# Kernel optimization log

Hardware: AMD Instinct MI355X
Metric: run time of the kernel (lower is better)

The kernel has to match this reference:

```python
import jax, jax.numpy as jnp
import numpy as np

IN_C = 256
INTER_C = 64  # in_c // k, k=4
B, H, W = 8, 32, 32
N_TERMS = 5   # numSeriesTerms; numTraceSamples = 1


def setup_inputs():
    key = jax.random.key(0)
    ks = jax.random.split(key, 10)
    s = 0.05
    return {
        "x": jax.random.normal(ks[0], (B, IN_C, H, W), jnp.float32),
        "Wq": jax.random.normal(ks[1], (INTER_C, IN_C), jnp.float32) * s,
        "bq": jax.random.normal(ks[2], (INTER_C,), jnp.float32) * s,
        "Wk": jax.random.normal(ks[3], (INTER_C, IN_C), jnp.float32) * s,
        "bk": jax.random.normal(ks[4], (INTER_C,), jnp.float32) * s,
        "Wc": jax.random.normal(ks[5], (2 * INTER_C,), jnp.float32) * s,
        "Wv": jax.random.normal(ks[6], (IN_C, IN_C), jnp.float32) * s,
        "bv": jax.random.normal(ks[7], (IN_C,), jnp.float32) * s,
        "gamma": jnp.full((1,), 0.5, jnp.float32),
        "u": jax.random.normal(ks[8], (B, IN_C, H, W), jnp.float32),
    }


def _attention(x, Wq, bq, Wk, bk, Wc, Wv, bv, gamma):
    # Attention_concat.forward. concat_conv is a bias-free linear map over the
    # channel concat, so energy[i,j] = <Wc[:ic], q_i> + <Wc[ic:], k_j> exactly.
    b, c, h, w = x.shape
    n = h * w
    xf = x.reshape(b, c, n)                                   # [B,C,N]
    q = jnp.einsum('oc,bcn->bon', Wq, xf) + bq[None, :, None]  # [B,ic,N]
    k = jnp.einsum('oc,bcn->bon', Wk, xf) + bk[None, :, None]  # [B,ic,N]
    ic = Wq.shape[0]
    eq = jnp.einsum('c,bcn->bn', Wc[:ic], q)                  # [B,N]
    ek = jnp.einsum('c,bcn->bn', Wc[ic:], k)                  # [B,N]
    attn = (eq[:, :, None] + ek[:, None, :]) / n              # energy/(H*W), [B,N,N]
    v = jnp.einsum('oc,bcn->bon', Wv, xf) + bv[None, :, None]  # [B,C,N]
    out = jnp.einsum('bcn,bnm->bcm', v, attn).reshape(b, c, h, w)
    return gamma * out + x


def _forward(x, Wq, bq, Wk, bk, Wc, Wv, bv, gamma, u):
    att = lambda z, g: _attention(z, Wq, bq, Wk, bk, Wc, Wv, bv, g)
    # turbulance_hook: runs under torch.no_grad and rescales gamma in-place
    res = att(x, gamma)
    turbu = att(x * 1.0000001, gamma)
    lip = jnp.linalg.norm(turbu - res) / jnp.linalg.norm(x * 1.0000001 - x)
    factor = jax.lax.stop_gradient(jnp.where(lip > 0.9, 0.9 / lip, 1.0))
    gamma_eff = gamma * factor
    Fx, vjp_fn = jax.vjp(lambda z: att(z, gamma_eff), x)
    # power_series_matrix_logarithm_trace: Hutchinson estimate of
    # tr(log(I+J)) ~= sum_j (-1)^{j+1}/j * u^T J^j u, 1 probe, 5 terms
    b = x.shape[0]
    uf = u.reshape(b, -1)
    vcur = u
    tr = jnp.zeros((b,), x.dtype)
    for j in range(1, N_TERMS + 1):
        vcur = vjp_fn(vcur)[0]                 # u^T J^j via repeated vjp
        dot = jnp.sum(vcur.reshape(b, -1) * uf, axis=1)
        tr = tr + ((-1.0) ** (j + 1) / j) * dot
    return x + Fx, tr


def reference(x, Wq, bq, Wk, bk, Wc, Wv, bv, gamma, u):
    return _forward(x, Wq, bq, Wk, bk, Wc, Wv, bv, gamma, u)
```

## Files before the change

### kernel.cpp

```cpp
#include <hip/hip_runtime.h>
#include <math.h>

#define NB 8
#define NC 256
#define NN 1024
#define NICH 64

#define WS_AQ    0
#define WS_AK    256
#define WS_CQ    512
#define WS_CK    513
#define WS_GE    514
#define WS_MOM   520
#define WS_SX    1024
#define WS_XE    3072
#define WS_XK    5120
#define WS_T1P   7424
#define WS_T2P   7488
#define WS_VSU   7680
#define WS_UE    9728
#define WS_VEU   11776
#define WS_CAQ   13824
#define WS_CAK   15872
#define WS_CUAK  17920
#define WS_STAT  20480
#define STAT_STRIDE 2560
#define ST_EQ    0
#define ST_EK    1024
#define ST_SV    2048
#define ST_SVE   2304
#define WS_MAQ   40960
#define WS_MAK   49152
#define WS_EQP   57344
#define WS_EKP   319488
#define WS_MAQP  581632
#define WS_MAKP  843776
#define WS_SX2P  1105920
#define WS_UUP   1106176

__device__ __forceinline__ float dot4(const float4& a, const float4& b) {
    return a.x * b.x + a.y * b.y + a.z * b.z + a.w * b.w;
}
__device__ __forceinline__ float sum4(const float4& a) {
    return a.x + a.y + a.z + a.w;
}

__global__ void k1(const float* __restrict__ x, const float* __restrict__ u,
                   const float* __restrict__ Wq, const float* __restrict__ bq,
                   const float* __restrict__ Wk, const float* __restrict__ bk,
                   const float* __restrict__ Wc, float* __restrict__ ws) {
    const int bid = blockIdx.x;
    const int b = bid >> 5, g = bid & 31;
    const int t = threadIdx.x;
    const int c0 = g * 8;
    const int wid = t >> 6, lane = t & 63;
    __shared__ float aql[8], akl[8];
    __shared__ float sxw[8][4];
    {
        const int c = t >> 5, i = t & 31;
        float a = Wc[i] * Wq[i * NC + c0 + c] + Wc[i + 32] * Wq[(i + 32) * NC + c0 + c];
        float k = Wc[64 + i] * Wk[i * NC + c0 + c] + Wc[96 + i] * Wk[(i + 32) * NC + c0 + c];
        for (int off = 16; off > 0; off >>= 1) {
            a += __shfl_down(a, off, 32);
            k += __shfl_down(k, off, 32);
        }
        if (i == 0) {
            aql[c] = a; akl[c] = k;
            ws[WS_AQ + c0 + c] = a;
            ws[WS_AK + c0 + c] = k;
        }
    }
    if (t < 64) {
        float p = Wc[t] * bq[t], r = Wc[64 + t] * bk[t];
        for (int off = 32; off > 0; off >>= 1) {
            p += __shfl_down(p, off, 64);
            r += __shfl_down(r, off, 64);
        }
        if (t == 0) { ws[WS_CQ] = p; ws[WS_CK] = r; }
    }
    __syncthreads();
    const float4* xb4 = (const float4*)(x + ((size_t)b * NC + c0) * NN);
    const float4* ub4 = (const float4*)(u + ((size_t)b * NC + c0) * NN);
    float4 eqp = {0.f, 0.f, 0.f, 0.f}, ekp = {0.f, 0.f, 0.f, 0.f};
    float4 map = {0.f, 0.f, 0.f, 0.f}, mkp = {0.f, 0.f, 0.f, 0.f};
#pragma unroll
    for (int c = 0; c < 8; ++c) {
        float4 xv = xb4[c * 256 + t];
        float4 uv = ub4[c * 256 + t];
        float a = aql[c], k = akl[c];
        eqp.x += a * xv.x; eqp.y += a * xv.y; eqp.z += a * xv.z; eqp.w += a * xv.w;
        ekp.x += k * xv.x; ekp.y += k * xv.y; ekp.z += k * xv.z; ekp.w += k * xv.w;
        map.x += a * uv.x; map.y += a * uv.y; map.z += a * uv.z; map.w += a * uv.w;
        mkp.x += k * uv.x; mkp.y += k * uv.y; mkp.z += k * uv.z; mkp.w += k * uv.w;
        float xs = sum4(xv);
        for (int off = 32; off > 0; off >>= 1) xs += __shfl_down(xs, off, 64);
        if (lane == 0) sxw[c][wid] = xs;
    }
    __syncthreads();
    if (t < 8) ws[WS_SX + b * NC + c0 + t] = sxw[t][0] + sxw[t][1] + sxw[t][2] + sxw[t][3];
    size_t pb = (size_t)bid * 1024;
    ((float4*)(ws + WS_EQP + pb))[t]  = eqp;
    ((float4*)(ws + WS_EKP + pb))[t]  = ekp;
    ((float4*)(ws + WS_MAQP + pb))[t] = map;
    ((float4*)(ws + WS_MAKP + pb))[t] = mkp;
}

__global__ void k2(float* __restrict__ ws) {
    const int bid = blockIdx.x;
    const int b = bid >> 2, qc = bid & 3;
    const int t = threadIdx.x;
    const int quarter = t >> 6, tn = t & 63;
    const int n4 = qc * 64 + tn;
    __shared__ float4 qb[4][4][64];
    float4 e4 = {0.f, 0.f, 0.f, 0.f}, k4 = {0.f, 0.f, 0.f, 0.f};
    float4 ma4 = {0.f, 0.f, 0.f, 0.f}, mk4 = {0.f, 0.f, 0.f, 0.f};
#pragma unroll
    for (int gg = 0; gg < 8; ++gg) {
        size_t pb = (size_t)(b * 32 + quarter * 8 + gg) * 1024;
        float4 v0 = ((const float4*)(ws + WS_EQP + pb))[n4];
        float4 v1 = ((const float4*)(ws + WS_EKP + pb))[n4];
        float4 v2 = ((const float4*)(ws + WS_MAQP + pb))[n4];
        float4 v3 = ((const float4*)(ws + WS_MAKP + pb))[n4];
        e4.x += v0.x; e4.y += v0.y; e4.z += v0.z; e4.w += v0.w;
        k4.x += v1.x; k4.y += v1.y; k4.z += v1.z; k4.w += v1.w;
        ma4.x += v2.x; ma4.y += v2.y; ma4.z += v2.z; ma4.w += v2.w;
        mk4.x += v3.x; mk4.y += v3.y; mk4.z += v3.z; mk4.w += v3.w;
    }
    qb[0][quarter][tn] = e4; qb[1][quarter][tn] = k4;
    qb[2][quarter][tn] = ma4; qb[3][quarter][tn] = mk4;
    __syncthreads();
    if (t < 64) {
        const float cq = ws[WS_CQ], ck = ws[WS_CK];
        float4 e = qb[0][0][t], kk = qb[1][0][t], ma = qb[2][0][t], mk = qb[3][0][t];
        for (int qq = 1; qq < 4; ++qq) {
            float4 a0 = qb[0][qq][t], a1 = qb[1][qq][t], a2 = qb[2][qq][t], a3 = qb[3][qq][t];
            e.x += a0.x; e.y += a0.y; e.z += a0.z; e.w += a0.w;
            kk.x += a1.x; kk.y += a1.y; kk.z += a1.z; kk.w += a1.w;
            ma.x += a2.x; ma.y += a2.y; ma.z += a2.z; ma.w += a2.w;
            mk.x += a3.x; mk.y += a3.y; mk.z += a3.z; mk.w += a3.w;
        }
        e.x += cq; e.y += cq; e.z += cq; e.w += cq;
        kk.x += ck; kk.y += ck; kk.z += ck; kk.w += ck;
        float* st = ws + WS_STAT + b * STAT_STRIDE;
        ((float4*)(st + ST_EQ))[n4] = e;
        ((float4*)(st + ST_EK))[n4] = kk;
        ((float4*)(ws + WS_MAQ + b * NN))[n4] = ma;
        ((float4*)(ws + WS_MAK + b * NN))[n4] = mk;
        float d0 = sum4(e);
        float d1 = sum4(kk);
        float d2 = dot4(kk, kk);
        float d3 = dot4(e, kk);
        for (int off = 32; off > 0; off >>= 1) {
            d0 += __shfl_down(d0, off, 64);
            d1 += __shfl_down(d1, off, 64);
            d2 += __shfl_down(d2, off, 64);
            d3 += __shfl_down(d3, off, 64);
        }
        if (t == 0) {
            ws[WS_MOM + bid * 4 + 0] = d0;
            ws[WS_MOM + bid * 4 + 1] = d1;
            ws[WS_MOM + bid * 4 + 2] = d2;
            ws[WS_MOM + bid * 4 + 3] = d3;
        }
    }
}

__global__ void k3(const float* __restrict__ x, const float* __restrict__ u,
                   float* __restrict__ ws) {
    const int bid = blockIdx.x;
    const int b = bid >> 5, g = bid & 31;
    const int t = threadIdx.x;
    const int c0 = g * 8;
    const int wid = t >> 6, lane = t & 63;
    __shared__ float wv8[8][8][4];
    __shared__ float accw[2][4];
    const float* st = ws + WS_STAT + b * STAT_STRIDE;
    float4 e4  = ((const float4*)(st + ST_EQ))[t];
    float4 k4v = ((const float4*)(st + ST_EK))[t];
    float4 ma4 = ((const float4*)(ws + WS_MAQ + b * NN))[t];
    float4 mk4 = ((const float4*)(ws + WS_MAK + b * NN))[t];
    const float4* xb4 = (const float4*)(x + ((size_t)b * NC + c0) * NN);
    const float4* ub4 = (const float4*)(u + ((size_t)b * NC + c0) * NN);
    float x2a = 0.f, uua = 0.f;
#pragma unroll
    for (int c = 0; c < 8; ++c) {
        float4 xv = xb4[c * 256 + t];
        float4 uv = ub4[c * 256 + t];
        float d[8];
        d[0] = dot4(xv, e4);
        d[1] = dot4(xv, k4v);
        d[2] = sum4(uv);
        d[3] = dot4(uv, e4);
        d[4] = dot4(uv, k4v);
        d[5] = dot4(xv, ma4);
        d[6] = dot4(xv, mk4);
        d[7] = dot4(uv, mk4);
        x2a += dot4(xv, xv);
        uua += dot4(uv, uv);
        for (int off = 32; off > 0; off >>= 1)
            for (int m = 0; m < 8; ++m) d[m] += __shfl_down(d[m], off, 64);
        if (lane == 0) for (int m = 0; m < 8; ++m) wv8[c][m][wid] = d[m];
    }
    for (int off = 32; off > 0; off >>= 1) {
        x2a += __shfl_down(x2a, off, 64);
        uua += __shfl_down(uua, off, 64);
    }
    if (lane == 0) { accw[0][wid] = x2a; accw[1][wid] = uua; }
    __syncthreads();
    if (t < 8) {
        int c = t;
        float v[8];
        for (int m = 0; m < 8; ++m)
            v[m] = wv8[c][m][0] + wv8[c][m][1] + wv8[c][m][2] + wv8[c][m][3];
        ws[WS_XE   + b * NC + c0 + c] = v[0];
        ws[WS_XK   + b * NC + c0 + c] = v[1];
        ws[WS_VSU  + b * NC + c0 + c] = v[2];
        ws[WS_UE   + b * NC + c0 + c] = v[3];
        ws[WS_VEU  + b * NC + c0 + c] = v[4];
        ws[WS_CAQ  + b * NC + c0 + c] = v[5];
        ws[WS_CAK  + b * NC + c0 + c] = v[6];
        ws[WS_CUAK + b * NC + c0 + c] = v[7];
    }
    if (t == 0) {
        ws[WS_SX2P + bid] = accw[0][0] + accw[0][1] + accw[0][2] + accw[0][3];
        ws[WS_UUP + bid]  = accw[1][0] + accw[1][1] + accw[1][2] + accw[1][3];
    }
}

__global__ void ksv(const float* __restrict__ Wv, const float* __restrict__ bv,
                    float* __restrict__ ws) {
    const int bid = blockIdx.x;
    const int b = bid >> 3, oc = bid & 7;
    const int t = threadIdx.x;
    const int o_sub = t >> 3, ks = t & 7;
    const int o = oc * 32 + o_sub;
    __shared__ float sxl[NC], xel[NC];
    __shared__ float T1s[32], T2s[32];
    sxl[t] = ws[WS_SX + b * NC + t];
    xel[t] = ws[WS_XE + b * NC + t];
    __syncthreads();
    float Seq = 0.f, Sek = 0.f, Sek2 = 0.f;
    for (int q = 0; q < 4; ++q) {
        Seq  += ws[WS_MOM + (b * 4 + q) * 4 + 0];
        Sek  += ws[WS_MOM + (b * 4 + q) * 4 + 1];
        Sek2 += ws[WS_MOM + (b * 4 + q) * 4 + 2];
    }
    const float cq = ws[WS_CQ], ck = ws[WS_CK];
    float wsx = 0.f, wxe = 0.f;
    const float4* wrow = (const float4*)(Wv + (size_t)o * NC);
#pragma unroll
    for (int i = 0; i < 8; ++i) {
        float4 w4 = wrow[i * 8 + ks];
        int k = i * 32 + ks * 4;
        wsx += w4.x * sxl[k] + w4.y * sxl[k + 1] + w4.z * sxl[k + 2] + w4.w * sxl[k + 3];
        wxe += w4.x * xel[k] + w4.y * xel[k + 1] + w4.z * xel[k + 2] + w4.w * xel[k + 3];
    }
    for (int off = 4; off > 0; off >>= 1) {
        wsx += __shfl_down(wsx, off, 8);
        wxe += __shfl_down(wxe, off, 8);
    }
    if (ks == 0) {
        float bvc = bv[o];
        float Sv  = wsx + (float)NN * bvc;
        float SvL = wsx;
        float Sve = wxe + bvc * Seq;
        float* st = ws + WS_STAT + b * STAT_STRIDE;
        st[ST_SV + o] = Sv; st[ST_SVE + o] = Sve;
        float A = 2.f * Sve - bvc * Seq - cq * Sv;
        float sx = sxl[o];
        float xk = ws[WS_XK + b * NC + o];
        float xkL = xk - ck * sx;
        float T1c = A * sx + Sv * xkL + SvL * xk;
        float SP  = Sek - (float)NN * ck;
        float SP2 = Sek2 - 2.f * ck * Sek + (float)NN * ck * ck;
        float SPQ = Sek2 - ck * Sek;
        float T2c = (float)NN * A * A + Sv * Sv * SP2 + SvL * SvL * Sek2
                  + 2.f * A * Sv * SP + 2.f * A * SvL * Sek + 2.f * Sv * SvL * SPQ;
        T1s[o_sub] = T1c; T2s[o_sub] = T2c;
    }
    __syncthreads();
    if (t == 0) {
        float t1 = 0.f, t2 = 0.f;
        for (int i = 0; i < 32; ++i) { t1 += T1s[i]; t2 += T2s[i]; }
        ws[WS_T1P + bid] = t1;
        ws[WS_T2P + bid] = t2;
    }
}

__global__ void kiter(
        const float* __restrict__ Wv, const float* __restrict__ bv,
        const float* __restrict__ gamma, float* __restrict__ ws,
        float* __restrict__ out) {
    const int b = blockIdx.x;
    const int t = threadIdx.x;
    const int o = t & 255, q = t >> 8;
    const int wid4 = o >> 6, lane = t & 63;
    __shared__ unsigned int Wlds[128 * 256];
    __shared__ float VV[2 * NC];
    __shared__ float redPR[2 * 1024];
    __shared__ float dred[9][4];
    __shared__ float gred0[4];
    __shared__ float gredT[2];
    __shared__ float sge;
#pragma unroll 4
    for (int r = 0; r < 32; ++r) {
        int c = r * 8 + q * 2;
        float w0 = Wv[(size_t)c * NC + o];
        float w1 = Wv[(size_t)(c + 1) * NC + o];
        unsigned int b0 = __float_as_uint(w0);
        unsigned int b1 = __float_as_uint(w1);
        b0 = (b0 + 0x7FFFu + ((b0 >> 16) & 1u)) >> 16;
        b1 = (b1 + 0x7FFFu + ((b1 >> 16) & 1u)) & 0xFFFF0000u;
        Wlds[(r * 4 + q) * 256 + o] = b0 | b1;
    }
    {
        float a = 0.f, b1 = 0.f, c1 = 0.f;
        if (t < 256) a = ws[WS_SX2P + t];
        if (t < 64) { b1 = ws[WS_T1P + t]; c1 = ws[WS_T2P + t]; }
        for (int off = 32; off > 0; off >>= 1) {
            a  += __shfl_down(a,  off, 64);
            b1 += __shfl_down(b1, off, 64);
            c1 += __shfl_down(c1, off, 64);
        }
        if (t < 256 && lane == 0) gred0[t >> 6] = a;
        if (t == 0) { gredT[0] = b1; gredT[1] = c1; }
    }
    __syncthreads();
    if (t == 0) {
        float S1 = gred0[0] + gred0[1] + gred0[2] + gred0[3];
        float T1 = gredT[0];
        float T2 = gredT[1];
        float inv = gamma[0] * (1.f / (float)NN);
        float dd = S1 + 2.f * inv * T1 + inv * inv * T2;
        float lip = sqrtf(dd / S1);
        float ge = gamma[0] * ((lip > 0.9f) ? (0.9f / lip) : 1.f);
        sge = ge;
        if (b == 0) ws[WS_GE] = ge;
    }
    __syncthreads();
    const float s = sge * (1.f / (float)NN);
    float Svl_r = 0.f, sxl_r = 0.f, xkl_r = 0.f, caql_r = 0.f, cakl_r = 0.f,
          Uel_r = 0.f, Vsul_r = 0.f, bvl_r = 0.f, aql_r = 0.f, akl_r = 0.f,
          veu_r = 0.f, cuak_r = 0.f, vsreg = 0.f, vereg = 0.f;
    if (t < 256) {
        const float* st = ws + WS_STAT + b * STAT_STRIDE;
        Svl_r  = st[ST_SV + t];
        sxl_r  = ws[WS_SX   + b * NC + t];
        xkl_r  = ws[WS_XK   + b * NC + t];
        caql_r = ws[WS_CAQ  + b * NC + t];
        cakl_r = ws[WS_CAK  + b * NC + t];
        Uel_r  = ws[WS_UE   + b * NC + t];
        Vsul_r = ws[WS_VSU  + b * NC + t];
        veu_r  = ws[WS_VEU  + b * NC + t];
        cuak_r = ws[WS_CUAK + b * NC + t];
        aql_r  = ws[WS_AQ + t];
        akl_r  = ws[WS_AK + t];
        bvl_r  = bv[t];
        vsreg = Vsul_r; vereg = veu_r;
        VV[2 * t] = vsreg; VV[2 * t + 1] = vereg;
    }
    float Seq = 0.f, Sek = 0.f, Sekq = 0.f;
    for (int qq = 0; qq < 4; ++qq) {
        Seq  += ws[WS_MOM + (b * 4 + qq) * 4 + 0];
        Sek  += ws[WS_MOM + (b * 4 + qq) * 4 + 1];
        Sekq += ws[WS_MOM + (b * 4 + qq) * 4 + 3];
    }
    float uu = 0.f;
    for (int g = 0; g < 32; ++g) uu += ws[WS_UUP + b * 32 + g];
    __syncthreads();
    if (t < 256) {
        float d[8] = {Svl_r * cuak_r, aql_r * Vsul_r, akl_r * Vsul_r, akl_r * Uel_r,
                      Svl_r * Vsul_r, Svl_r * veu_r,  Svl_r * aql_r,  Svl_r * akl_r};
        for (int off = 32; off > 0; off >>= 1)
            for (int m = 0; m < 8; ++m) d[m] += __shfl_down(d[m], off, 64);
        if (lane == 0) for (int m = 0; m < 8; ++m) dred[m][wid4] = d[m];
    }
    __syncthreads();
    float g2a = 0.f, aqVsu = 0.f, akVsu = 0.f, akUe = 0.f, SvVsu = 0.f, SvVeu = 0.f,
          Svaq = 0.f, Svak = 0.f;
    if (t < 256) {
        g2a   = dred[0][0] + dred[0][1] + dred[0][2] + dred[0][3];
        aqVsu = dred[1][0] + dred[1][1] + dred[1][2] + dred[1][3];
        akVsu = dred[2][0] + dred[2][1] + dred[2][2] + dred[2][3];
        akUe  = dred[3][0] + dred[3][1] + dred[3][2] + dred[3][3];
        SvVsu = dred[4][0] + dred[4][1] + dred[4][2] + dred[4][3];
        SvVeu = dred[5][0] + dred[5][1] + dred[5][2] + dred[5][3];
        Svaq  = dred[6][0] + dred[6][1] + dred[6][2] + dred[6][3];
        Svak  = dred[7][0] + dred[7][1] + dred[7][2] + dred[7][3];
    }
    __syncthreads();
    const float lam = 1.f + s * Svak;
    float alpha = 1.f, beta = 0.f, gam = 0.f;
    float SxAcc = 0.f, XkAcc = 0.f, CakAcc = 0.f;
    float dot = uu, tr = 0.f;
    const float coef[5] = {1.f, -0.5f, 1.f / 3.f, -0.25f, 0.2f};
    for (int j = 0; j < 5; ++j) {
        float pa = 0.f, ra = 0.f;
#pragma unroll
        for (int ii = 0; ii < 32; ++ii) {
            int i = q * 32 + ii;
            unsigned int w = Wlds[i * 256 + o];
            float4 vv = ((const float4*)VV)[i];
            float wlo = __uint_as_float(w << 16);
            float whi = __uint_as_float(w & 0xFFFF0000u);
            pa += wlo * vv.x + whi * vv.z;
            ra += wlo * vv.y + whi * vv.w;
        }
        redPR[2 * t] = pa; redPR[2 * t + 1] = ra;
        __syncthreads();
        float Pv = 0.f, Rv = 0.f;
        if (t < 256) {
            Pv = s * (redPR[2 * t] + redPR[2 * (t + 256)] + redPR[2 * (t + 512)] + redPR[2 * (t + 768)]);
            Rv = s * (redPR[2 * t + 1] + redPR[2 * (t + 256) + 1] + redPR[2 * (t + 512) + 1] + redPR[2 * (t + 768) + 1]);
            float d[9];
            d[0] = Svl_r * Pv;
            d[1] = Svl_r * Rv;
            d[2] = bvl_r * vsreg;
            d[3] = sxl_r * Pv;
            d[4] = xkl_r * Pv;
            d[5] = caql_r * Pv;
            d[6] = cakl_r * Pv;
            d[7] = Uel_r * Pv;
            d[8] = Vsul_r * Rv;
            for (int off = 32; off > 0; off >>= 1)
                for (int m = 0; m < 9; ++m) d[m] += __shfl_down(d[m], off, 64);
            if (lane == 0) for (int m = 0; m < 9; ++m) dred[m][wid4] = d[m];
        }
        __syncthreads();
        if (t < 256) {
            float sm[9];
            for (int m = 0; m < 9; ++m) sm[m] = dred[m][0] + dred[m][1] + dred[m][2] + dred[m][3];
            const float svP = sm[0], svR = sm[1], bvVs = sm[2], sxP = sm[3], xkP = sm[4],
                        caqP = sm[5], cakP = sm[6], ueP = sm[7], vsuR = sm[8];
            const float sB = s * bvVs;
            float St  = s * (alpha * SvVsu + beta * (float)NN + gam * Seq  + Svaq * SxAcc);
            float tek = s * (alpha * SvVeu + beta * Sek        + gam * Sekq + Svaq * XkAcc);
            float uta = s * (alpha * g2a   + beta * akVsu      + gam * akUe + Svaq * CakAcc);
            dot += ueP + caqP + sB * aqVsu + uta + vsuR;
            tr  += coef[j] * dot;
            float nVs = vsreg + Pv * Seq  + aql_r * (sxP + (float)NN * sB) + akl_r * St  + Rv * (float)NN;
            float nVe = vereg + Pv * Sekq + aql_r * (xkP + sB * Sek)       + akl_r * tek + Rv * Sek;
            vsreg = nVs; vereg = nVe;
            VV[2 * t] = nVs; VV[2 * t + 1] = nVe;
            SxAcc  = lam * SxAcc  + sxP;
            XkAcc  = lam * XkAcc  + xkP;
            CakAcc = lam * CakAcc + cakP;
            beta = lam * beta + Svaq * sB + svR;
            gam  = lam * gam + svP;
            alpha *= lam;
        }
        __syncthreads();
    }
    if (t == 0) out[2097152 + b] = tr;
}

__global__ void kout0(const float* __restrict__ x, const float* __restrict__ ws,
                      float* __restrict__ out) {
    int bid = blockIdx.x;
    int b = bid >> 8, c = bid & 255, t = threadIdx.x;
    float ge = ws[WS_GE] * (1.f / (float)NN);
    const float* st = ws + WS_STAT + b * STAT_STRIDE;
    float sv = st[ST_SV + c], sve = st[ST_SVE + c];
    float4 ek4 = ((const float4*)(st + ST_EK))[t];
    size_t i4 = (size_t)bid * 256 + t;
    float4 x4 = ((const float4*)x)[i4];
    float4 o;
    o.x = 2.f * x4.x + ge * (sve + ek4.x * sv);
    o.y = 2.f * x4.y + ge * (sve + ek4.y * sv);
    o.z = 2.f * x4.z + ge * (sve + ek4.z * sv);
    o.w = 2.f * x4.w + ge * (sve + ek4.w * sv);
    ((float4*)out)[i4] = o;
}

extern "C" void kernel_launch(void* const* d_in, const int* in_sizes, int n_in,
                              void* d_out, int out_size, void* d_ws, size_t ws_size,
                              hipStream_t stream) {
    const float* x     = (const float*)d_in[0];
    const float* Wq    = (const float*)d_in[1];
    const float* bq    = (const float*)d_in[2];
    const float* Wk    = (const float*)d_in[3];
    const float* bk    = (const float*)d_in[4];
    const float* Wc    = (const float*)d_in[5];
    const float* Wv    = (const float*)d_in[6];
    const float* bv    = (const float*)d_in[7];
    const float* gamma = (const float*)d_in[8];
    const float* u     = (const float*)d_in[9];
    float* out = (float*)d_out;
    float* ws  = (float*)d_ws;

    k1   <<<dim3(256),  dim3(256),  0, stream>>>(x, u, Wq, bq, Wk, bk, Wc, ws);
    k2   <<<dim3(32),   dim3(256),  0, stream>>>(ws);
    k3   <<<dim3(256),  dim3(256),  0, stream>>>(x, u, ws);
    ksv  <<<dim3(64),   dim3(256),  0, stream>>>(Wv, bv, ws);
    kiter<<<dim3(8),    dim3(1024), 0, stream>>>(Wv, bv, gamma, ws, out);
    kout0<<<dim3(2048), dim3(256),  0, stream>>>(x, ws, out);
}
```

Before: 55.15 us.

## Fuse six kernels into one cooperative megakernel with grid syncs

Replaces the six separate launches with a single cooperative kernel of 256 blocks. Phases are separated by grid.sync(), and their shared memory is reused through one union buffer. The serial iteration phase now runs on 256 threads per block instead of 1024, with Wv staged into LDS as packed bf16 using a different layout. This removes launch gaps between the small kernels, but costs grid-wide barriers and less parallelism in the iteration and output phases, since the final output pass now runs on 256 blocks rather than 2048.

```diff
diff --git a/kernel.cpp b/kernel.cpp
--- a/kernel.cpp
+++ b/kernel.cpp
@@ -1,5 +1,8 @@
 #include <hip/hip_runtime.h>
+#include <hip/hip_cooperative_groups.h>
 #include <math.h>
+
+namespace cg = cooperative_groups;
 
 #define NB 8
 #define NC 256
@@ -44,432 +47,446 @@
 __device__ __forceinline__ float sum4(const float4& a) {
     return a.x + a.y + a.z + a.w;
 }
-
-__global__ void k1(const float* __restrict__ x, const float* __restrict__ u,
-                   const float* __restrict__ Wq, const float* __restrict__ bq,
-                   const float* __restrict__ Wk, const float* __restrict__ bk,
-                   const float* __restrict__ Wc, float* __restrict__ ws) {
+__device__ __forceinline__ unsigned int bf16lo(float v) {
+    unsigned int u = __float_as_uint(v);
+    return (u + 0x7FFFu + ((u >> 16) & 1u)) >> 16;
+}
+__device__ __forceinline__ unsigned int bf16hi(float v) {
+    unsigned int u = __float_as_uint(v);
+    return (u + 0x7FFFu + ((u >> 16) & 1u)) & 0xFFFF0000u;
+}
+
+struct SMemP5 {
+    unsigned int Wlds2[256][128];
+    float VV[512];
+    float redM[256][8];
+    float dred[9][4];
+    float gred0[4];
+    float gredT[2];
+    float sge;
+};
+struct SMemP1 { float aql[8], akl[8]; float sxw[8][4]; };
+struct SMemP2 { float4 qb[4][4][64]; };
+struct SMemP3 { float wv8[8][8][4]; float accw[2][4]; };
+struct SMemP4 { float sxl[NC], xel[NC]; float T1s[32], T2s[32]; };
+
+__global__ void __launch_bounds__(256) mega(
+        const float* __restrict__ x, const float* __restrict__ u,
+        const float* __restrict__ Wq, const float* __restrict__ bq,
+        const float* __restrict__ Wk, const float* __restrict__ bk,
+        const float* __restrict__ Wc, const float* __restrict__ Wv,
+        const float* __restrict__ bv, const float* __restrict__ gamma,
+        float* __restrict__ ws, float* __restrict__ out) {
+    cg::grid_group grid = cg::this_grid();
+    __shared__ __align__(16) unsigned char smem_raw[sizeof(SMemP5)];
     const int bid = blockIdx.x;
-    const int b = bid >> 5, g = bid & 31;
     const int t = threadIdx.x;
-    const int c0 = g * 8;
     const int wid = t >> 6, lane = t & 63;
-    __shared__ float aql[8], akl[8];
-    __shared__ float sxw[8][4];
+
     {
-        const int c = t >> 5, i = t & 31;
-        float a = Wc[i] * Wq[i * NC + c0 + c] + Wc[i + 32] * Wq[(i + 32) * NC + c0 + c];
-        float k = Wc[64 + i] * Wk[i * NC + c0 + c] + Wc[96 + i] * Wk[(i + 32) * NC + c0 + c];
-        for (int off = 16; off > 0; off >>= 1) {
-            a += __shfl_down(a, off, 32);
-            k += __shfl_down(k, off, 32);
-        }
-        if (i == 0) {
-            aql[c] = a; akl[c] = k;
-            ws[WS_AQ + c0 + c] = a;
-            ws[WS_AK + c0 + c] = k;
-        }
+        SMemP1& S = *(SMemP1*)smem_raw;
+        const int b = bid >> 5, g = bid & 31;
+        const int c0 = g * 8;
+        {
+            const int c = t >> 5, i = t & 31;
+            float a = Wc[i] * Wq[i * NC + c0 + c] + Wc[i + 32] * Wq[(i + 32) * NC + c0 + c];
+            float k = Wc[64 + i] * Wk[i * NC + c0 + c] + Wc[96 + i] * Wk[(i + 32) * NC + c0 + c];
+            for (int off = 16; off > 0; off >>= 1) {
+                a += __shfl_down(a, off, 32);
+                k += __shfl_down(k, off, 32);
+            }
+            if (i == 0) {
+                S.aql[c] = a; S.akl[c] = k;
+                ws[WS_AQ + c0 + c] = a;
+                ws[WS_AK + c0 + c] = k;
+            }
+        }
+        if (t < 64) {
+            float p = Wc[t] * bq[t], r = Wc[64 + t] * bk[t];
+            for (int off = 32; off > 0; off >>= 1) {
+                p += __shfl_down(p, off, 64);
+                r += __shfl_down(r, off, 64);
+            }
+            if (t == 0) { ws[WS_CQ] = p; ws[WS_CK] = r; }
+        }
+        __syncthreads();
+        const float4* xb4 = (const float4*)(x + ((size_t)b * NC + c0) * NN);
+        const float4* ub4 = (const float4*)(u + ((size_t)b * NC + c0) * NN);
+        float4 eqp = {0.f, 0.f, 0.f, 0.f}, ekp = {0.f, 0.f, 0.f, 0.f};
+        float4 map = {0.f, 0.f, 0.f, 0.f}, mkp = {0.f, 0.f, 0.f, 0.f};
+#pragma unroll
+        for (int c = 0; c < 8; ++c) {
+            float4 xv = xb4[c * 256 + t];
+            float4 uv = ub4[c * 256 + t];
+            float a = S.aql[c], k = S.akl[c];
+            eqp.x += a * xv.x; eqp.y += a * xv.y; eqp.z += a * xv.z; eqp.w += a * xv.w;
+            ekp.x += k * xv.x; ekp.y += k * xv.y; ekp.z += k * xv.z; ekp.w += k * xv.w;
+            map.x += a * uv.x; map.y += a * uv.y; map.z += a * uv.z; map.w += a * uv.w;
+            mkp.x += k * uv.x; mkp.y += k * uv.y; mkp.z += k * uv.z; mkp.w += k * uv.w;
+            float xs = sum4(xv);
+            for (int off = 32; off > 0; off >>= 1) xs += __shfl_down(xs, off, 64);
+            if (lane == 0) S.sxw[c][wid] = xs;
+        }
+        __syncthreads();
+        if (t < 8) ws[WS_SX + b * NC + c0 + t] = S.sxw[t][0] + S.sxw[t][1] + S.sxw[t][2] + S.sxw[t][3];
+        size_t pb = (size_t)bid * 1024;
+        ((float4*)(ws + WS_EQP + pb))[t]  = eqp;
+        ((float4*)(ws + WS_EKP + pb))[t]  = ekp;
+        ((float4*)(ws + WS_MAQP + pb))[t] = map;
+        ((float4*)(ws + WS_MAKP + pb))[t] = mkp;
     }
-    if (t < 64) {
-        float p = Wc[t] * bq[t], r = Wc[64 + t] * bk[t];
+    grid.sync();
+
+    if (bid < 32) {
+        SMemP2& S = *(SMemP2*)smem_raw;
+        const int b = bid >> 2, qc = bid & 3;
+        const int quarter = t >> 6, tn = t & 63;
+        const int n4 = qc * 64 + tn;
+        float4 e4 = {0.f, 0.f, 0.f, 0.f}, k4 = {0.f, 0.f, 0.f, 0.f};
+        float4 ma4 = {0.f, 0.f, 0.f, 0.f}, mk4 = {0.f, 0.f, 0.f, 0.f};
+#pragma unroll
+        for (int gg = 0; gg < 8; ++gg) {
+            size_t pb = (size_t)(b * 32 + quarter * 8 + gg) * 1024;
+            float4 v0 = ((const float4*)(ws + WS_EQP + pb))[n4];
+            float4 v1 = ((const float4*)(ws + WS_EKP + pb))[n4];
+            float4 v2 = ((const float4*)(ws + WS_MAQP + pb))[n4];
+            float4 v3 = ((const float4*)(ws + WS_MAKP + pb))[n4];
+            e4.x += v0.x; e4.y += v0.y; e4.z += v0.z; e4.w += v0.w;
+            k4.x += v1.x; k4.y += v1.y; k4.z += v1.z; k4.w += v1.w;
+            ma4.x += v2.x; ma4.y += v2.y; ma4.z += v2.z; ma4.w += v2.w;
+            mk4.x += v3.x; mk4.y += v3.y; mk4.z += v3.z; mk4.w += v3.w;
+        }
+        S.qb[0][quarter][tn] = e4; S.qb[1][quarter][tn] = k4;
+        S.qb[2][quarter][tn] = ma4; S.qb[3][quarter][tn] = mk4;
+        __syncthreads();
+        if (t < 64) {
+            const float cq = ws[WS_CQ], ck = ws[WS_CK];
+            float4 e = S.qb[0][0][t], kk = S.qb[1][0][t], ma = S.qb[2][0][t], mk = S.qb[3][0][t];
+            for (int qq = 1; qq < 4; ++qq) {
+                float4 a0 = S.qb[0][qq][t], a1 = S.qb[1][qq][t], a2 = S.qb[2][qq][t], a3 = S.qb[3][qq][t];
+                e.x += a0.x; e.y += a0.y; e.z += a0.z; e.w += a0.w;
+                kk.x += a1.x; kk.y += a1.y; kk.z += a1.z; kk.w += a1.w;
+                ma.x += a2.x; ma.y += a2.y; ma.z += a2.z; ma.w += a2.w;
+                mk.x += a3.x; mk.y += a3.y; mk.z += a3.z; mk.w += a3.w;
+            }
+            e.x += cq; e.y += cq; e.z += cq; e.w += cq;
+            kk.x += ck; kk.y += ck; kk.z += ck; kk.w += ck;
+            float* st = ws + WS_STAT + b * STAT_STRIDE;
+            ((float4*)(st + ST_EQ))[n4] = e;
+            ((float4*)(st + ST_EK))[n4] = kk;
+            ((float4*)(ws + WS_MAQ + b * NN))[n4] = ma;
+            ((float4*)(ws + WS_MAK + b * NN))[n4] = mk;
+            float d0 = sum4(e);
+            float d1 = sum4(kk);
+            float d2 = dot4(kk, kk);
+            float d3 = dot4(e, kk);
+            for (int off = 32; off > 0; off >>= 1) {
+                d0 += __shfl_down(d0, off, 64);
+                d1 += __shfl_down(d1, off, 64);
+                d2 += __shfl_down(d2, off, 64);
+                d3 += __shfl_down(d3, off, 64);
+            }
+            if (t == 0) {
+                ws[WS_MOM + bid * 4 + 0] = d0;
+                ws[WS_MOM + bid * 4 + 1] = d1;
+                ws[WS_MOM + bid * 4 + 2] = d2;
+                ws[WS_MOM + bid * 4 + 3] = d3;
+            }
+        }
+    }
+    grid.sync();
+
+    {
+        SMemP3& S = *(SMemP3*)smem_raw;
+        const int b = bid >> 5, g = bid & 31;
+        const int c0 = g * 8;
+        const float* st = ws + WS_STAT + b * STAT_STRIDE;
+        float4 e4  = ((const float4*)(st + ST_EQ))[t];
+        float4 k4v = ((const float4*)(st + ST_EK))[t];
+        float4 ma4 = ((const float4*)(ws + WS_MAQ + b * NN))[t];
+        float4 mk4 = ((const float4*)(ws + WS_MAK + b * NN))[t];
+        const float4* xb4 = (const float4*)(x + ((size_t)b * NC + c0) * NN);
+        const float4* ub4 = (const float4*)(u + ((size_t)b * NC + c0) * NN);
+        float x2a = 0.f, uua = 0.f;
+#pragma unroll
+        for (int c = 0; c < 8; ++c) {
+            float4 xv = xb4[c * 256 + t];
+            float4 uv = ub4[c * 256 + t];
+            float d[8];
+            d[0] = dot4(xv, e4);
+            d[1] = dot4(xv, k4v);
+            d[2] = sum4(uv);
+            d[3] = dot4(uv, e4);
+            d[4] = dot4(uv, k4v);
+            d[5] = dot4(xv, ma4);
+            d[6] = dot4(xv, mk4);
+            d[7] = dot4(uv, mk4);
+            x2a += dot4(xv, xv);
+            uua += dot4(uv, uv);
+            for (int off = 32; off > 0; off >>= 1)
+                for (int m = 0; m < 8; ++m) d[m] += __shfl_down(d[m], off, 64);
+            if (lane == 0) for (int m = 0; m < 8; ++m) S.wv8[c][m][wid] = d[m];
+        }
         for (int off = 32; off > 0; off >>= 1) {
-            p += __shfl_down(p, off, 64);
-            r += __shfl_down(r, off, 64);
-        }
-        if (t == 0) { ws[WS_CQ] = p; ws[WS_CK] = r; }
+            x2a += __shfl_down(x2a, off, 64);
+            uua += __shfl_down(uua, off, 64);
+        }
+        if (lane == 0) { S.accw[0][wid] = x2a; S.accw[1][wid] = uua; }
+        __syncthreads();
+        if (t < 8) {
+            int c = t;
+            float v[8];
+            for (int m = 0; m < 8; ++m)
+                v[m] = S.wv8[c][m][0] + S.wv8[c][m][1] + S.wv8[c][m][2] + S.wv8[c][m][3];
+            ws[WS_XE   + b * NC + c0 + c] = v[0];
+            ws[WS_XK   + b * NC + c0 + c] = v[1];
+            ws[WS_VSU  + b * NC + c0 + c] = v[2];
+            ws[WS_UE   + b * NC + c0 + c] = v[3];
+            ws[WS_VEU  + b * NC + c0 + c] = v[4];
+            ws[WS_CAQ  + b * NC + c0 + c] = v[5];
+            ws[WS_CAK  + b * NC + c0 + c] = v[6];
+            ws[WS_CUAK + b * NC + c0 + c] = v[7];
+        }
+        if (t == 0) {
+            ws[WS_SX2P + bid] = S.accw[0][0] + S.accw[0][1] + S.accw[0][2] + S.accw[0][3];
+            ws[WS_UUP + bid]  = S.accw[1][0] + S.accw[1][1] + S.accw[1][2] + S.accw[1][3];
+        }
     }
-    __syncthreads();
-    const float4* xb4 = (const float4*)(x + ((size_t)b * NC + c0) * NN);
-    const float4* ub4 = (const float4*)(u + ((size_t)b * NC + c0) * NN);
-    float4 eqp = {0.f, 0.f, 0.f, 0.f}, ekp = {0.f, 0.f, 0.f, 0.f};
-    float4 map = {0.f, 0.f, 0.f, 0.f}, mkp = {0.f, 0.f, 0.f, 0.f};
+    grid.sync();
+
+    if (bid < 64) {
+        SMemP4& S = *(SMemP4*)smem_raw;
+        const int b = bid >> 3, oc = bid & 7;
+        const int o_sub = t >> 3, ks = t & 7;
+        const int o = oc * 32 + o_sub;
+        S.sxl[t] = ws[WS_SX + b * NC + t];
+        S.xel[t] = ws[WS_XE + b * NC + t];
+        __syncthreads();
+        float Seq = 0.f, Sek = 0.f, Sek2 = 0.f;
+        for (int q = 0; q < 4; ++q) {
+            Seq  += ws[WS_MOM + (b * 4 + q) * 4 + 0];
+            Sek  += ws[WS_MOM + (b * 4 + q) * 4 + 1];
+            Sek2 += ws[WS_MOM + (b * 4 + q) * 4 + 2];
+        }
+        const float cq = ws[WS_CQ], ck = ws[WS_CK];
+        float wsx = 0.f, wxe = 0.f;
+        const float4* wrow = (const float4*)(Wv + (size_t)o * NC);
 #pragma unroll
-    for (int c = 0; c < 8; ++c) {
-        float4 xv = xb4[c * 256 + t];
-        float4 uv = ub4[c * 256 + t];
-        float a = aql[c], k = akl[c];
-        eqp.x += a * xv.x; eqp.y += a * xv.y; eqp.z += a * xv.z; eqp.w += a * xv.w;
-        ekp.x += k * xv.x; ekp.y += k * xv.y; ekp.z += k * xv.z; ekp.w += k * xv.w;
-        map.x += a * uv.x; map.y += a * uv.y; map.z += a * uv.z; map.w += a * uv.w;
-        mkp.x += k * uv.x; mkp.y += k * uv.y; mkp.z += k * uv.z; mkp.w += k * uv.w;
-        float xs = sum4(xv);
-        for (int off = 32; off > 0; off >>= 1) xs += __shfl_down(xs, off, 64);
-        if (lane == 0) sxw[c][wid] = xs;
+        for (int i = 0; i < 8; ++i) {
+            float4 w4 = wrow[i * 8 + ks];
+            int k = i * 32 + ks * 4;
+            wsx += w4.x * S.sxl[k] + w4.y * S.sxl[k + 1] + w4.z * S.sxl[k + 2] + w4.w * S.sxl[k + 3];
+            wxe += w4.x * S.xel[k] + w4.y * S.xel[k + 1] + w4.z * S.xel[k + 2] + w4.w * S.xel[k + 3];
+        }
+        for (int off = 4; off > 0; off >>= 1) {
+            wsx += __shfl_down(wsx, off, 8);
+            wxe += __shfl_down(wxe, off, 8);
+        }
+        if (ks == 0) {
+            float bvc = bv[o];
+            float Sv  = wsx + (float)NN * bvc;
+            float SvL = wsx;
+            float Sve = wxe + bvc * Seq;
+            float* st = ws + WS_STAT + b * STAT_STRIDE;
+            st[ST_SV + o] = Sv; st[ST_SVE + o] = Sve;
+            float A = 2.f * Sve - bvc * Seq - cq * Sv;
+            float sx = S.sxl[o];
+            float xk = ws[WS_XK + b * NC + o];
+            float xkL = xk - ck * sx;
+            float T1c = A * sx + Sv * xkL + SvL * xk;
+            float SP  = Sek - (float)NN * ck;
+            float SP2 = Sek2 - 2.f * ck * Sek + (float)NN * ck * ck;
+            float SPQ = Sek2 - ck * Sek;
+            float T2c = (float)NN * A * A + Sv * Sv * SP2 + SvL * SvL * Sek2
+                      + 2.f * A * Sv * SP + 2.f * A * SvL * Sek + 2.f * Sv * SvL * SPQ;
+            S.T1s[o_sub] = T1c; S.T2s[o_sub] = T2c;
+        }
+        __syncthreads();
+        if (t == 0) {
+            float t1 = 0.f, t2 = 0.f;
+            for (int i = 0; i < 32; ++i) { t1 += S.T1s[i]; t2 += S.T2s[i]; }
+            ws[WS_T1P + bid] = t1;
+            ws[WS_T2P + bid] = t2;
+        }
     }
-    __syncthreads();
-    if (t < 8) ws[WS_SX + b * NC + c0 + t] = sxw[t][0] + sxw[t][1] + sxw[t][2] + sxw[t][3];
-    size_t pb = (size_t)bid * 1024;
-    ((float4*)(ws + WS_EQP + pb))[t]  = eqp;
-    ((float4*)(ws + WS_EKP + pb))[t]  = ekp;
-    ((float4*)(ws + WS_MAQP + pb))[t] = map;
-    ((float4*)(ws + WS_MAKP + pb))[t] = mkp;
-}
-
-__global__ void k2(float* __restrict__ ws) {
-    const int bid = blockIdx.x;
-    const int b = bid >> 2, qc = bid & 3;
-    const int t = threadIdx.x;
-    const int quarter = t >> 6, tn = t & 63;
-    const int n4 = qc * 64 + tn;
-    __shared__ float4 qb[4][4][64];
-    float4 e4 = {0.f, 0.f, 0.f, 0.f}, k4 = {0.f, 0.f, 0.f, 0.f};
-    float4 ma4 = {0.f, 0.f, 0.f, 0.f}, mk4 = {0.f, 0.f, 0.f, 0.f};
+    grid.sync();
+
+    if (bid < NB) {
+        SMemP5& S = *(SMemP5*)smem_raw;
+        const int b = bid;
+        const float4* Wv4 = (const float4*)Wv;
+#pragma unroll 8
+        for (int r = 0; r < 64; ++r) {
+            int gidx = r * 256 + t;
+            float4 f = Wv4[gidx];
+            int c = gidx >> 6, m = gidx & 63;
+            S.Wlds2[c][2 * m]     = bf16lo(f.x) | bf16hi(f.y);
+            S.Wlds2[c][2 * m + 1] = bf16lo(f.z) | bf16hi(f.w);
+        }
+        {
+            float a = ws[WS_SX2P + t];
+            float b1 = 0.f, c1 = 0.f;
+            if (t < 64) { b1 = ws[WS_T1P + t]; c1 = ws[WS_T2P + t]; }
+            for (int off = 32; off > 0; off >>= 1) {
+                a  += __shfl_down(a,  off, 64);
+                b1 += __shfl_down(b1, off, 64);
+                c1 += __shfl_down(c1, off, 64);
+            }
+            if (lane == 0) S.gred0[wid] = a;
+            if (t == 0) { S.gredT[0] = b1; S.gredT[1] = c1; }
+        }
+        __syncthreads();
+        if (t == 0) {
+            float S1 = S.gred0[0] + S.gred0[1] + S.gred0[2] + S.gred0[3];
+            float inv = gamma[0] * (1.f / (float)NN);
+            float dd = S1 + 2.f * inv * S.gredT[0] + inv * inv * S.gredT[1];
+            float lip = sqrtf(dd / S1);
+            float ge = gamma[0] * ((lip > 0.9f) ? (0.9f / lip) : 1.f);
+            S.sge = ge;
+            if (b == 0) ws[WS_GE] = ge;
+        }
+        __syncthreads();
+        const float s = S.sge * (1.f / (float)NN);
+        const float* st = ws + WS_STAT + b * STAT_STRIDE;
+        float Svl_r  = st[ST_SV + t];
+        float sxl_r  = ws[WS_SX   + b * NC + t];
+        float xkl_r  = ws[WS_XK   + b * NC + t];
+        float caql_r = ws[WS_CAQ  + b * NC + t];
+        float cakl_r = ws[WS_CAK  + b * NC + t];
+        float Uel_r  = ws[WS_UE   + b * NC + t];
+        float Vsul_r = ws[WS_VSU  + b * NC + t];
+        float veu_r  = ws[WS_VEU  + b * NC + t];
+        float cuak_r = ws[WS_CUAK + b * NC + t];
+        float aql_r  = ws[WS_AQ + t];
+        float akl_r  = ws[WS_AK + t];
+        float bvl_r  = bv[t];
+        float vsreg = Vsul_r, vereg = veu_r;
+        S.VV[2 * t] = vsreg; S.VV[2 * t + 1] = vereg;
+        float Seq = 0.f, Sek = 0.f, Sekq = 0.f;
+        for (int qq = 0; qq < 4; ++qq) {
+            Seq  += ws[WS_MOM + (b * 4 + qq) * 4 + 0];
+            Sek  += ws[WS_MOM + (b * 4 + qq) * 4 + 1];
+            Sekq += ws[WS_MOM + (b * 4 + qq) * 4 + 3];
+        }
+        float uu = 0.f;
+        for (int g = 0; g < 32; ++g) uu += ws[WS_UUP + b * 32 + g];
+        __syncthreads();
+        {
+            float d[8] = {Svl_r * cuak_r, aql_r * Vsul_r, akl_r * Vsul_r, akl_r * Uel_r,
+                          Svl_r * Vsul_r, Svl_r * veu_r,  Svl_r * aql_r,  Svl_r * akl_r};
+            for (int off = 32; off > 0; off >>= 1)
+                for (int m = 0; m < 8; ++m) d[m] += __shfl_down(d[m], off, 64);
+            if (lane == 0) for (int m = 0; m < 8; ++m) S.dred[m][wid] = d[m];
+        }
+        __syncthreads();
+        const float g2a   = S.dred[0][0] + S.dred[0][1] + S.dred[0][2] + S.dred[0][3];
+        const float aqVsu = S.dred[1][0] + S.dred[1][1] + S.dred[1][2] + S.dred[1][3];
+        const float akVsu = S.dred[2][0] + S.dred[2][1] + S.dred[2][2] + S.dred[2][3];
+        const float akUe  = S.dred[3][0] + S.dred[3][1] + S.dred[3][2] + S.dred[3][3];
+        const float SvVsu = S.dred[4][0] + S.dred[4][1] + S.dred[4][2] + S.dred[4][3];
+        const float SvVeu = S.dred[5][0] + S.dred[5][1] + S.dred[5][2] + S.dred[5][3];
+        const float Svaq  = S.dred[6][0] + S.dred[6][1] + S.dred[6][2] + S.dred[6][3];
+        const float Svak  = S.dred[7][0] + S.dred[7][1] + S.dred[7][2] + S.dred[7][3];
+        __syncthreads();
+        const float lam = 1.f + s * Svak;
+        float alpha = 1.f, beta = 0.f, gam = 0.f;
+        float SxAcc = 0.f, XkAcc = 0.f, CakAcc = 0.f;
+        float dot = uu, tr = 0.f;
+        const float coef[5] = {1.f, -0.5f, 1.f / 3.f, -0.25f, 0.2f};
+        const int q4 = t & 63, cqh = t >> 6;
+        for (int j = 0; j < 5; ++j) {
+            float pa0 = 0.f, pa1 = 0.f, pa2 = 0.f, pa3 = 0.f;
+            float ra0 = 0.f, ra1 = 0.f, ra2 = 0.f, ra3 = 0.f;
+#pragma unroll 16
+            for (int i = 0; i < 64; ++i) {
+                int c = cqh * 64 + i;
+                uint2 w2 = *(const uint2*)&S.Wlds2[c][2 * q4];
+                float2 vv = *(const float2*)&S.VV[2 * c];
+                float w0 = __uint_as_float(w2.x << 16);
+                float w1 = __uint_as_float(w2.x & 0xFFFF0000u);
+                float w2f = __uint_as_float(w2.y << 16);
+                float w3 = __uint_as_float(w2.y & 0xFFFF0000u);
+                pa0 += w0 * vv.x;  ra0 += w0 * vv.y;
+                pa1 += w1 * vv.x;  ra1 += w1 * vv.y;
+                pa2 += w2f * vv.x; ra2 += w2f * vv.y;
+                pa3 += w3 * vv.x;  ra3 += w3 * vv.y;
+            }
+            S.redM[t][0] = pa0; S.redM[t][1] = pa1; S.redM[t][2] = pa2; S.redM[t][3] = pa3;
+            S.redM[t][4] = ra0; S.redM[t][5] = ra1; S.redM[t][6] = ra2; S.redM[t][7] = ra3;
+            __syncthreads();
+            float Pv, Rv;
+            {
+                int q4o = t >> 2, r = t & 3;
+                float pa = S.redM[q4o][r] + S.redM[64 + q4o][r]
+                         + S.redM[128 + q4o][r] + S.redM[192 + q4o][r];
+                float ra = S.redM[q4o][4 + r] + S.redM[64 + q4o][4 + r]
+                         + S.redM[128 + q4o][4 + r] + S.redM[192 + q4o][4 + r];
+                Pv = s * pa; Rv = s * ra;
+            }
+            {
+                float d[9];
+                d[0] = Svl_r * Pv;
+                d[1] = Svl_r * Rv;
+                d[2] = bvl_r * vsreg;
+                d[3] = sxl_r * Pv;
+                d[4] = xkl_r * Pv;
+                d[5] = caql_r * Pv;
+                d[6] = cakl_r * Pv;
+                d[7] = Uel_r * Pv;
+                d[8] = Vsul_r * Rv;
+                for (int off = 32; off > 0; off >>= 1)
+                    for (int m = 0; m < 9; ++m) d[m] += __shfl_down(d[m], off, 64);
+                if (lane == 0) for (int m = 0; m < 9; ++m) S.dred[m][wid] = d[m];
+            }
+            __syncthreads();
+            {
+                float sm[9];
+                for (int m = 0; m < 9; ++m)
+                    sm[m] = S.dred[m][0] + S.dred[m][1] + S.dred[m][2] + S.dred[m][3];
+                const float svP = sm[0], svR = sm[1], bvVs = sm[2], sxP = sm[3], xkP = sm[4],
+                            caqP = sm[5], cakP = sm[6], ueP = sm[7], vsuR = sm[8];
+                const float sB = s * bvVs;
+                float St  = s * (alpha * SvVsu + beta * (float)NN + gam * Seq  + Svaq * SxAcc);
+                float tek = s * (alpha * SvVeu + beta * Sek        + gam * Sekq + Svaq * XkAcc);
+                float uta = s * (alpha * g2a   + beta * akVsu      + gam * akUe + Svaq * CakAcc);
+                dot += ueP + caqP + sB * aqVsu + uta + vsuR;
+                tr  += coef[j] * dot;
+                float nVs = vsreg + Pv * Seq  + aql_r * (sxP + (float)NN * sB) + akl_r * St  + Rv * (float)NN;
+                float nVe = vereg + Pv * Sekq + aql_r * (xkP + sB * Sek)       + akl_r * tek + Rv * Sek;
+                vsreg = nVs; vereg = nVe;
+                S.VV[2 * t] = nVs; S.VV[2 * t + 1] = nVe;
+                SxAcc  = lam * SxAcc  + sxP;
+                XkAcc  = lam * XkAcc  + xkP;
+                CakAcc = lam * CakAcc + cakP;
+                beta = lam * beta + Svaq * sB + svR;
+                gam  = lam * gam + svP;
+                alpha *= lam;
+            }
+            __syncthreads();
+        }
+        if (t == 0) out[2097152 + b] = tr;
+    }
+    grid.sync();
+
+    {
+        const float ge = ws[WS_GE] * (1.f / (float)NN);
 #pragma unroll
-    for (int gg = 0; gg < 8; ++gg) {
-        size_t pb = (size_t)(b * 32 + quarter * 8 + gg) * 1024;
-        float4 v0 = ((const float4*)(ws + WS_EQP + pb))[n4];
-        float4 v1 = ((const float4*)(ws + WS_EKP + pb))[n4];
-        float4 v2 = ((const float4*)(ws + WS_MAQP + pb))[n4];
-        float4 v3 = ((const float4*)(ws + WS_MAKP + pb))[n4];
-        e4.x += v0.x; e4.y += v0.y; e4.z += v0.z; e4.w += v0.w;
-        k4.x += v1.x; k4.y += v1.y; k4.z += v1.z; k4.w += v1.w;
-        ma4.x += v2.x; ma4.y += v2.y; ma4.z += v2.z; ma4.w += v2.w;
-        mk4.x += v3.x; mk4.y += v3.y; mk4.z += v3.z; mk4.w += v3.w;
+        for (int it = 0; it < 8; ++it) {
+            int bid2 = it * 256 + bid;
+            int b = bid2 >> 8, c = bid2 & 255;
+            const float* st = ws + WS_STAT + b * STAT_STRIDE;
+            float sv = st[ST_SV + c], sve = st[ST_SVE + c];
+            float4 ek4 = ((const float4*)(st + ST_EK))[t];
+            size_t i4 = (size_t)bid2 * 256 + t;
+            float4 x4 = ((const float4*)x)[i4];
+            float4 o;
+            o.x = 2.f * x4.x + ge * (sve + ek4.x * sv);
+            o.y = 2.f * x4.y + ge * (sve + ek4.y * sv);
+            o.z = 2.f * x4.z + ge * (sve + ek4.z * sv);
+            o.w = 2.f * x4.w + ge * (sve + ek4.w * sv);
+            ((float4*)out)[i4] = o;
+        }
     }
-    qb[0][quarter][tn] = e4; qb[1][quarter][tn] = k4;
-    qb[2][quarter][tn] = ma4; qb[3][quarter][tn] = mk4;
-    __syncthreads();
-    if (t < 64) {
-        const float cq = ws[WS_CQ], ck = ws[WS_CK];
-        float4 e = qb[0][0][t], kk = qb[1][0][t], ma = qb[2][0][t], mk = qb[3][0][t];
-        for (int qq = 1; qq < 4; ++qq) {
-            float4 a0 = qb[0][qq][t], a1 = qb[1][qq][t], a2 = qb[2][qq][t], a3 = qb[3][qq][t];
-            e.x += a0.x; e.y += a0.y; e.z += a0.z; e.w += a0.w;
-            kk.x += a1.x; kk.y += a1.y; kk.z += a1.z; kk.w += a1.w;
-            ma.x += a2.x; ma.y += a2.y; ma.z += a2.z; ma.w += a2.w;
-            mk.x += a3.x; mk.y += a3.y; mk.z += a3.z; mk.w += a3.w;
-        }
-        e.x += cq; e.y += cq; e.z += cq; e.w += cq;
-        kk.x += ck; kk.y += ck; kk.z += ck; kk.w += ck;
-        float* st = ws + WS_STAT + b * STAT_STRIDE;
-        ((float4*)(st + ST_EQ))[n4] = e;
-        ((float4*)(st + ST_EK))[n4] = kk;
-        ((float4*)(ws + WS_MAQ + b * NN))[n4] = ma;
-        ((float4*)(ws + WS_MAK + b * NN))[n4] = mk;
-        float d0 = sum4(e);
-        float d1 = sum4(kk);
-        float d2 = dot4(kk, kk);
-        float d3 = dot4(e, kk);
-        for (int off = 32; off > 0; off >>= 1) {
-            d0 += __shfl_down(d0, off, 64);
-            d1 += __shfl_down(d1, off, 64);
-            d2 += __shfl_down(d2, off, 64);
-            d3 += __shfl_down(d3, off, 64);
-        }
-        if (t == 0) {
-            ws[WS_MOM + bid * 4 + 0] = d0;
-            ws[WS_MOM + bid * 4 + 1] = d1;
-            ws[WS_MOM + bid * 4 + 2] = d2;
-            ws[WS_MOM + bid * 4 + 3] = d3;
-        }
-    }
-}
-
-__global__ void k3(const float* __restrict__ x, const float* __restrict__ u,
-                   float* __restrict__ ws) {
-    const int bid = blockIdx.x;
-    const int b = bid >> 5, g = bid & 31;
-    const int t = threadIdx.x;
-    const int c0 = g * 8;
-    const int wid = t >> 6, lane = t & 63;
-    __shared__ float wv8[8][8][4];
-    __shared__ float accw[2][4];
-    const float* st = ws + WS_STAT + b * STAT_STRIDE;
-    float4 e4  = ((const float4*)(st + ST_EQ))[t];
-    float4 k4v = ((const float4*)(st + ST_EK))[t];
-    float4 ma4 = ((const float4*)(ws + WS_MAQ + b * NN))[t];
-    float4 mk4 = ((const float4*)(ws + WS_MAK + b * NN))[t];
-    const float4* xb4 = (const float4*)(x + ((size_t)b * NC + c0) * NN);
-    const float4* ub4 = (const float4*)(u + ((size_t)b * NC + c0) * NN);
-    float x2a = 0.f, uua = 0.f;
-#pragma unroll
-    for (int c = 0; c < 8; ++c) {
-        float4 xv = xb4[c * 256 + t];
-        float4 uv = ub4[c * 256 + t];
-        float d[8];
-        d[0] = dot4(xv, e4);
-        d[1] = dot4(xv, k4v);
-        d[2] = sum4(uv);
-        d[3] = dot4(uv, e4);
-        d[4] = dot4(uv, k4v);
-        d[5] = dot4(xv, ma4);
-        d[6] = dot4(xv, mk4);
-        d[7] = dot4(uv, mk4);
-        x2a += dot4(xv, xv);
-        uua += dot4(uv, uv);
-        for (int off = 32; off > 0; off >>= 1)
-            for (int m = 0; m < 8; ++m) d[m] += __shfl_down(d[m], off, 64);
-        if (lane == 0) for (int m = 0; m < 8; ++m) wv8[c][m][wid] = d[m];
-    }
-    for (int off = 32; off > 0; off >>= 1) {
-        x2a += __shfl_down(x2a, off, 64);
-        uua += __shfl_down(uua, off, 64);
-    }
-    if (lane == 0) { accw[0][wid] = x2a; accw[1][wid] = uua; }
-    __syncthreads();
-    if (t < 8) {
-        int c = t;
-        float v[8];
-        for (int m = 0; m < 8; ++m)
-            v[m] = wv8[c][m][0] + wv8[c][m][1] + wv8[c][m][2] + wv8[c][m][3];
-        ws[WS_XE   + b * NC + c0 + c] = v[0];
-        ws[WS_XK   + b * NC + c0 + c] = v[1];
-        ws[WS_VSU  + b * NC + c0 + c] = v[2];
-        ws[WS_UE   + b * NC + c0 + c] = v[3];
-        ws[WS_VEU  + b * NC + c0 + c] = v[4];
-        ws[WS_CAQ  + b * NC + c0 + c] = v[5];
-        ws[WS_CAK  + b * NC + c0 + c] = v[6];
-        ws[WS_CUAK + b * NC + c0 + c] = v[7];
-    }
-    if (t == 0) {
-        ws[WS_SX2P + bid] = accw[0][0] + accw[0][1] + accw[0][2] + accw[0][3];
-        ws[WS_UUP + bid]  = accw[1][0] + accw[1][1] + accw[1][2] + accw[1][3];
-    }
-}
-
-__global__ void ksv(const float* __restrict__ Wv, const float* __restrict__ bv,
-                    float* __restrict__ ws) {
-    const int bid = blockIdx.x;
-    const int b = bid >> 3, oc = bid & 7;
-    const int t = threadIdx.x;
-    const int o_sub = t >> 3, ks = t & 7;
-    const int o = oc * 32 + o_sub;
-    __shared__ float sxl[NC], xel[NC];
-    __shared__ float T1s[32], T2s[32];
-    sxl[t] = ws[WS_SX + b * NC + t];
-    xel[t] = ws[WS_XE + b * NC + t];
-    __syncthreads();
-    float Seq = 0.f, Sek = 0.f, Sek2 = 0.f;
-    for (int q = 0; q < 4; ++q) {
-        Seq  += ws[WS_MOM + (b * 4 + q) * 4 + 0];
-        Sek  += ws[WS_MOM + (b * 4 + q) * 4 + 1];
-        Sek2 += ws[WS_MOM + (b * 4 + q) * 4 + 2];
-    }
-    const float cq = ws[WS_CQ], ck = ws[WS_CK];
-    float wsx = 0.f, wxe = 0.f;
-    const float4* wrow = (const float4*)(Wv + (size_t)o * NC);
-#pragma unroll
-    for (int i = 0; i < 8; ++i) {
-        float4 w4 = wrow[i * 8 + ks];
-        int k = i * 32 + ks * 4;
-        wsx += w4.x * sxl[k] + w4.y * sxl[k + 1] + w4.z * sxl[k + 2] + w4.w * sxl[k + 3];
-        wxe += w4.x * xel[k] + w4.y * xel[k + 1] + w4.z * xel[k + 2] + w4.w * xel[k + 3];
-    }
-    for (int off = 4; off > 0; off >>= 1) {
-        wsx += __shfl_down(wsx, off, 8);
-        wxe += __shfl_down(wxe, off, 8);
-    }
-    if (ks == 0) {
-        float bvc = bv[o];
-        float Sv  = wsx + (float)NN * bvc;
-        float SvL = wsx;
-        float Sve = wxe + bvc * Seq;
-        float* st = ws + WS_STAT + b * STAT_STRIDE;
-        st[ST_SV + o] = Sv; st[ST_SVE + o] = Sve;
-        float A = 2.f * Sve - bvc * Seq - cq * Sv;
-        float sx = sxl[o];
-        float xk = ws[WS_XK + b * NC + o];
-        float xkL = xk - ck * sx;
-        float T1c = A * sx + Sv * xkL + SvL * xk;
-        float SP  = Sek - (float)NN * ck;
-        float SP2 = Sek2 - 2.f * ck * Sek + (float)NN * ck * ck;
-        float SPQ = Sek2 - ck * Sek;
-        float T2c = (float)NN * A * A + Sv * Sv * SP2 + SvL * SvL * Sek2
-                  + 2.f * A * Sv * SP + 2.f * A * SvL * Sek + 2.f * Sv * SvL * SPQ;
-        T1s[o_sub] = T1c; T2s[o_sub] = T2c;
-    }
-    __syncthreads();
-    if (t == 0) {
-        float t1 = 0.f, t2 = 0.f;
-        for (int i = 0; i < 32; ++i) { t1 += T1s[i]; t2 += T2s[i]; }
-        ws[WS_T1P + bid] = t1;
-        ws[WS_T2P + bid] = t2;
-    }
-}
-
-__global__ void kiter(
-        const float* __restrict__ Wv, const float* __restrict__ bv,
-        const float* __restrict__ gamma, float* __restrict__ ws,
-        float* __restrict__ out) {
-    const int b = blockIdx.x;
-    const int t = threadIdx.x;
-    const int o = t & 255, q = t >> 8;
-    const int wid4 = o >> 6, lane = t & 63;
-    __shared__ unsigned int Wlds[128 * 256];
-    __shared__ float VV[2 * NC];
-    __shared__ float redPR[2 * 1024];
-    __shared__ float dred[9][4];
-    __shared__ float gred0[4];
-    __shared__ float gredT[2];
-    __shared__ float sge;
-#pragma unroll 4
-    for (int r = 0; r < 32; ++r) {
-        int c = r * 8 + q * 2;
-        float w0 = Wv[(size_t)c * NC + o];
-        float w1 = Wv[(size_t)(c + 1) * NC + o];
-        unsigned int b0 = __float_as_uint(w0);
-        unsigned int b1 = __float_as_uint(w1);
-        b0 = (b0 + 0x7FFFu + ((b0 >> 16) & 1u)) >> 16;
-        b1 = (b1 + 0x7FFFu + ((b1 >> 16) & 1u)) & 0xFFFF0000u;
-        Wlds[(r * 4 + q) * 256 + o] = b0 | b1;
-    }
-    {
-        float a = 0.f, b1 = 0.f, c1 = 0.f;
-        if (t < 256) a = ws[WS_SX2P + t];
-        if (t < 64) { b1 = ws[WS_T1P + t]; c1 = ws[WS_T2P + t]; }
-        for (int off = 32; off > 0; off >>= 1) {
-            a  += __shfl_down(a,  off, 64);
-            b1 += __shfl_down(b1, off, 64);
-            c1 += __shfl_down(c1, off, 64);
-        }
-        if (t < 256 && lane == 0) gred0[t >> 6] = a;
-        if (t == 0) { gredT[0] = b1; gredT[1] = c1; }
-    }
-    __syncthreads();
-    if (t == 0) {
-        float S1 = gred0[0] + gred0[1] + gred0[2] + gred0[3];
-        float T1 = gredT[0];
-        float T2 = gredT[1];
-        float inv = gamma[0] * (1.f / (float)NN);
-        float dd = S1 + 2.f * inv * T1 + inv * inv * T2;
-        float lip = sqrtf(dd / S1);
-        float ge = gamma[0] * ((lip > 0.9f) ? (0.9f / lip) : 1.f);
-        sge = ge;
-        if (b == 0) ws[WS_GE] = ge;
-    }
-    __syncthreads();
-    const float s = sge * (1.f / (float)NN);
-    float Svl_r = 0.f, sxl_r = 0.f, xkl_r = 0.f, caql_r = 0.f, cakl_r = 0.f,
-          Uel_r = 0.f, Vsul_r = 0.f, bvl_r = 0.f, aql_r = 0.f, akl_r = 0.f,
-          veu_r = 0.f, cuak_r = 0.f, vsreg = 0.f, vereg = 0.f;
-    if (t < 256) {
-        const float* st = ws + WS_STAT + b * STAT_STRIDE;
-        Svl_r  = st[ST_SV + t];
-        sxl_r  = ws[WS_SX   + b * NC + t];
-        xkl_r  = ws[WS_XK   + b * NC + t];
-        caql_r = ws[WS_CAQ  + b * NC + t];
-        cakl_r = ws[WS_CAK  + b * NC + t];
-        Uel_r  = ws[WS_UE   + b * NC + t];
-        Vsul_r = ws[WS_VSU  + b * NC + t];
-        veu_r  = ws[WS_VEU  + b * NC + t];
-        cuak_r = ws[WS_CUAK + b * NC + t];
-        aql_r  = ws[WS_AQ + t];
-        akl_r  = ws[WS_AK + t];
-        bvl_r  = bv[t];
-        vsreg = Vsul_r; vereg = veu_r;
-        VV[2 * t] = vsreg; VV[2 * t + 1] = vereg;
-    }
-    float Seq = 0.f, Sek = 0.f, Sekq = 0.f;
-    for (int qq = 0; qq < 4; ++qq) {
-        Seq  += ws[WS_MOM + (b * 4 + qq) * 4 + 0];
-        Sek  += ws[WS_MOM + (b * 4 + qq) * 4 + 1];
-        Sekq += ws[WS_MOM + (b * 4 + qq) * 4 + 3];
-    }
-    float uu = 0.f;
-    for (int g = 0; g < 32; ++g) uu += ws[WS_UUP + b * 32 + g];
-    __syncthreads();
-    if (t < 256) {
-        float d[8] = {Svl_r * cuak_r, aql_r * Vsul_r, akl_r * Vsul_r, akl_r * Uel_r,
-                      Svl_r * Vsul_r, Svl_r * veu_r,  Svl_r * aql_r,  Svl_r * akl_r};
-        for (int off = 32; off > 0; off >>= 1)
-            for (int m = 0; m < 8; ++m) d[m] += __shfl_down(d[m], off, 64);
-        if (lane == 0) for (int m = 0; m < 8; ++m) dred[m][wid4] = d[m];
-    }
-    __syncthreads();
-    float g2a = 0.f, aqVsu = 0.f, akVsu = 0.f, akUe = 0.f, SvVsu = 0.f, SvVeu = 0.f,
-          Svaq = 0.f, Svak = 0.f;
-    if (t < 256) {
-        g2a   = dred[0][0] + dred[0][1] + dred[0][2] + dred[0][3];
-        aqVsu = dred[1][0] + dred[1][1] + dred[1][2] + dred[1][3];
-        akVsu = dred[2][0] + dred[2][1] + dred[2][2] + dred[2][3];
-        akUe  = dred[3][0] + dred[3][1] + dred[3][2] + dred[3][3];
-        SvVsu = dred[4][0] + dred[4][1] + dred[4][2] + dred[4][3];
-        SvVeu = dred[5][0] + dred[5][1] + dred[5][2] + dred[5][3];
-        Svaq  = dred[6][0] + dred[6][1] + dred[6][2] + dred[6][3];
-        Svak  = dred[7][0] + dred[7][1] + dred[7][2] + dred[7][3];
-    }
-    __syncthreads();
-    const float lam = 1.f + s * Svak;
-    float alpha = 1.f, beta = 0.f, gam = 0.f;
-    float SxAcc = 0.f, XkAcc = 0.f, CakAcc = 0.f;
-    float dot = uu, tr = 0.f;
-    const float coef[5] = {1.f, -0.5f, 1.f / 3.f, -0.25f, 0.2f};
-    for (int j = 0; j < 5; ++j) {
-        float pa = 0.f, ra = 0.f;
-#pragma unroll
-        for (int ii = 0; ii < 32; ++ii) {
-            int i = q * 32 + ii;
-            unsigned int w = Wlds[i * 256 + o];
-            float4 vv = ((const float4*)VV)[i];
-            float wlo = __uint_as_float(w << 16);
-            float whi = __uint_as_float(w & 0xFFFF0000u);
-            pa += wlo * vv.x + whi * vv.z;
-            ra += wlo * vv.y + whi * vv.w;
-        }
-        redPR[2 * t] = pa; redPR[2 * t + 1] = ra;
-        __syncthreads();
-        float Pv = 0.f, Rv = 0.f;
-        if (t < 256) {
-            Pv = s * (redPR[2 * t] + redPR[2 * (t + 256)] + redPR[2 * (t + 512)] + redPR[2 * (t + 768)]);
-            Rv = s * (redPR[2 * t + 1] + redPR[2 * (t + 256) + 1] + redPR[2 * (t + 512) + 1] + redPR[2 * (t + 768) + 1]);
-            float d[9];
-            d[0] = Svl_r * Pv;
-            d[1] = Svl_r * Rv;
-            d[2] = bvl_r * vsreg;
-            d[3] = sxl_r * Pv;
-            d[4] = xkl_r * Pv;
-            d[5] = caql_r * Pv;
-            d[6] = cakl_r * Pv;
-            d[7] = Uel_r * Pv;
-            d[8] = Vsul_r * Rv;
-            for (int off = 32; off > 0; off >>= 1)
-                for (int m = 0; m < 9; ++m) d[m] += __shfl_down(d[m], off, 64);
-            if (lane == 0) for (int m = 0; m < 9; ++m) dred[m][wid4] = d[m];
-        }
-        __syncthreads();
-        if (t < 256) {
-            float sm[9];
-            for (int m = 0; m < 9; ++m) sm[m] = dred[m][0] + dred[m][1] + dred[m][2] + dred[m][3];
-            const float svP = sm[0], svR = sm[1], bvVs = sm[2], sxP = sm[3], xkP = sm[4],
-                        caqP = sm[5], cakP = sm[6], ueP = sm[7], vsuR = sm[8];
-            const float sB = s * bvVs;
-            float St  = s * (alpha * SvVsu + beta * (float)NN + gam * Seq  + Svaq * SxAcc);
-            float tek = s * (alpha * SvVeu + beta * Sek        + gam * Sekq + Svaq * XkAcc);
-            float uta = s * (alpha * g2a   + beta * akVsu      + gam * akUe + Svaq * CakAcc);
-            dot += ueP + caqP + sB * aqVsu + uta + vsuR;
-            tr  += coef[j] * dot;
-            float nVs = vsreg + Pv * Seq  + aql_r * (sxP + (float)NN * sB) + akl_r * St  + Rv * (float)NN;
-            float nVe = vereg + Pv * Sekq + aql_r * (xkP + sB * Sek)       + akl_r * tek + Rv * Sek;
-            vsreg = nVs; vereg = nVe;
-            VV[2 * t] = nVs; VV[2 * t + 1] = nVe;
-            SxAcc  = lam * SxAcc  + sxP;
-            XkAcc  = lam * XkAcc  + xkP;
-            CakAcc = lam * CakAcc + cakP;
-            beta = lam * beta + Svaq * sB + svR;
-            gam  = lam * gam + svP;
-            alpha *= lam;
-        }
-        __syncthreads();
-    }
-    if (t == 0) out[2097152 + b] = tr;
-}
-
-__global__ void kout0(const float* __restrict__ x, const float* __restrict__ ws,
-                      float* __restrict__ out) {
-    int bid = blockIdx.x;
-    int b = bid >> 8, c = bid & 255, t = threadIdx.x;
-    float ge = ws[WS_GE] * (1.f / (float)NN);
-    const float* st = ws + WS_STAT + b * STAT_STRIDE;
-    float sv = st[ST_SV + c], sve = st[ST_SVE + c];
-    float4 ek4 = ((const float4*)(st + ST_EK))[t];
-    size_t i4 = (size_t)bid * 256 + t;
-    float4 x4 = ((const float4*)x)[i4];
-    float4 o;
-    o.x = 2.f * x4.x + ge * (sve + ek4.x * sv);
-    o.y = 2.f * x4.y + ge * (sve + ek4.y * sv);
-    o.z = 2.f * x4.z + ge * (sve + ek4.z * sv);
-    o.w = 2.f * x4.w + ge * (sve + ek4.w * sv);
-    ((float4*)out)[i4] = o;
 }
 
 extern "C" void kernel_launch(void* const* d_in, const int* in_sizes, int n_in,
@@ -488,10 +505,8 @@
     float* out = (float*)d_out;
     float* ws  = (float*)d_ws;
 
-    k1   <<<dim3(256),  dim3(256),  0, stream>>>(x, u, Wq, bq, Wk, bk, Wc, ws);
-    k2   <<<dim3(32),   dim3(256),  0, stream>>>(ws);
-    k3   <<<dim3(256),  dim3(256),  0, stream>>>(x, u, ws);
-    ksv  <<<dim3(64),   dim3(256),  0, stream>>>(Wv, bv, ws);
-    kiter<<<dim3(8),    dim3(1024), 0, stream>>>(Wv, bv, gamma, ws, out);
-    kout0<<<dim3(2048), dim3(256),  0, stream>>>(x, ws, out);
+    void* args[] = {(void*)&x, (void*)&u, (void*)&Wq, (void*)&bq, (void*)&Wk,
+                    (void*)&bk, (void*)&Wc, (void*)&Wv, (void*)&bv, (void*)&gamma,
+                    (void*)&ws, (void*)&out};
+    hipLaunchCooperativeKernel((void*)mega, dim3(256), dim3(256), args, 0, stream);
 }
```

Result: slower. 198.7 us (+260.3%).
